# Kernel tuning notes

Hardware: AMD Instinct MI355X
Metric: run time of the kernel (lower is better)

Reference implementation:

```python
import jax, jax.numpy as jnp
import numpy as np

B, S, D, H = 4, 2048, 1024, 16
HD = D // H  # head_dim = 64


def setup_inputs() -> dict:
    key = jax.random.key(0)
    ks = jax.random.split(key, 6)
    scale = 0.02
    x = jax.random.normal(ks[0], (B, S, D), dtype=jnp.float32)
    # per-head projection weights, torch Linear is y = x @ W.T; store as [H, D, HD]
    Wq = jax.random.normal(ks[1], (H, D, HD), dtype=jnp.float32) * scale
    Wk = jax.random.normal(ks[2], (H, D, HD), dtype=jnp.float32) * scale
    Wv = jax.random.normal(ks[3], (H, D, HD), dtype=jnp.float32) * scale
    Wo = jax.random.normal(ks[4], (D, D), dtype=jnp.float32) * scale  # torch [out, in]
    bo = jax.random.normal(ks[5], (D,), dtype=jnp.float32) * scale
    return {"x": x, "Wq": Wq, "Wk": Wk, "Wv": Wv, "Wo": Wo, "bo": bo}


def reference(x, Wq, Wk, Wv, Wo, bo):
    # project: [B,S,D] x [H,D,HD] -> [B,H,S,HD]
    q = jnp.einsum("bsd,hde->bhse", x, Wq)
    k = jnp.einsum("bsd,hde->bhse", x, Wk)
    v = jnp.einsum("bsd,hde->bhse", x, Wv)
    scores = jnp.einsum("bhse,bhte->bhst", q, k) / jnp.sqrt(jnp.float32(HD))
    causal = jnp.tril(jnp.ones((S, S), dtype=bool))  # same as registered tril mask
    scores = jnp.where(causal, scores, -jnp.inf)
    w = jax.nn.softmax(scores, axis=-1)
    out = jnp.einsum("bhst,bhte->bhse", w, v)  # [B,H,S,HD]
    # concat heads along feature dim: [B,S,H*HD] = [B,S,D]
    out = out.transpose(0, 2, 1, 3).reshape(B, S, D)
    # output projection: torch Linear y = x @ W.T + b
    return jnp.einsum("bsd,od->bso", out, Wo) + bo
```

## Files before the change

kernel.cpp:

```cpp
#include <hip/hip_runtime.h>
#include <hip/hip_bf16.h>

typedef __bf16 bf16x8 __attribute__((ext_vector_type(8)));
typedef float f32x4 __attribute__((ext_vector_type(4)));
typedef unsigned short u16x4 __attribute__((ext_vector_type(4)));
typedef unsigned short u16x8 __attribute__((ext_vector_type(8)));
typedef unsigned uint4v __attribute__((ext_vector_type(4)));

#define B_ 4
#define S_ 2048
#define D_ 1024
#define H_ 16
#define HD_ 64

__device__ __forceinline__ unsigned short f2bf(float f) {
  unsigned u = __float_as_uint(f);
  u += 0x7fff + ((u >> 16) & 1);
  return (unsigned short)(u >> 16);
}

__device__ __forceinline__ void gload16(const void* g, void* l) {
  __builtin_amdgcn_global_load_lds((const __attribute__((address_space(1))) unsigned int*)g,
                                   (__attribute__((address_space(3))) unsigned int*)l,
                                   16, 0, 0);
}

__global__ void pack_x_k(const float* __restrict__ in, unsigned short* __restrict__ out, int n4) {
  int i = blockIdx.x * blockDim.x + threadIdx.x;
  int stride = gridDim.x * blockDim.x;
  for (; i < n4; i += stride) {
    float4 v = reinterpret_cast<const float4*>(in)[i];
    u16x4 o = {f2bf(v.x), f2bf(v.y), f2bf(v.z), f2bf(v.w)};
    reinterpret_cast<u16x4*>(out)[i] = o;
  }
}

__global__ void pack_wqkv_k(const float* __restrict__ Wq, const float* __restrict__ Wk,
                            const float* __restrict__ Wv, unsigned short* __restrict__ Wt) {
  int o = blockIdx.x * blockDim.x + threadIdx.x;
  int n = o >> 10;
  int d = o & 1023;
  const float* W = (n < 1024) ? Wq : (n < 2048) ? Wk : Wv;
  int nn = n & 1023;
  int h = nn >> 6, e = nn & 63;
  Wt[o] = f2bf(W[(h << 16) + (d << 6) + e]);
}

__global__ __launch_bounds__(512, 2) void gemm256_k(const unsigned short* __restrict__ A,
                                                    const unsigned short* __restrict__ Bt,
                                                    unsigned short* __restrict__ QK,
                                                    unsigned short* __restrict__ VT,
                                                    int M, int N, int K) {
  __shared__ __align__(16) unsigned short lA0[2][128 * 64];
  __shared__ __align__(16) unsigned short lA1[2][128 * 64];
  __shared__ __align__(16) unsigned short lB[2][192 * 64];
  const int tid = threadIdx.x;
  const int wid = tid >> 6, lane = tid & 63;
  const int r = lane & 15, g = lane >> 4;
  const int wm = wid >> 2, wn = wid & 3;

  const int i_hw = blockIdx.y * gridDim.x + blockIdx.x;
  const int xcd = i_hw & 7, j = i_hw >> 3;
  const long arow0 = (long)((xcd & 3) * 8 + (j & 7)) * 256;
  const long bcol0 = (long)((xcd >> 2) * 8 + (j >> 3)) * 192;

  const f32x4 z4 = {0.f, 0.f, 0.f, 0.f};
  f32x4 acc[8][3];
#pragma unroll
  for (int m = 0; m < 8; ++m)
#pragma unroll
    for (int n = 0; n < 3; ++n) acc[m][n] = z4;

  auto stage_half = [&](int kt, int which) {
    const unsigned short* src = (which == 2) ? Bt + bcol0 * K : A + (arow0 + 128 * which) * K;
    const int k0 = kt << 6;
    unsigned short* base = (which == 0) ? &lA0[kt & 1][0]
                         : (which == 1) ? &lA1[kt & 1][0] : &lB[kt & 1][0];
    const int nch = (which == 2) ? 3 : 2;
    for (int c = 0; c < nch; ++c) {
      const int jj = c * 512 + tid;
      const int row = jj >> 3, cc = jj & 7;
      const int ccs = cc ^ (row & 7);
      gload16(src + (long)row * K + k0 + ccs * 8, base + jj * 8);
    }
  };

  bf16x8 af[4][2], bv[3][2];
  auto read_a = [&](const unsigned short* lbase) {
#pragma unroll
    for (int i2 = 0; i2 < 4; ++i2)
#pragma unroll
      for (int kk = 0; kk < 2; ++kk) {
        const int rowh = (2 * i2 + wm) * 16 + r;
        af[i2][kk] = *(const bf16x8*)&lbase[rowh * 64 + (((kk << 2) + g) ^ (rowh & 7)) * 8];
      }
  };
  auto read_b = [&](int buf) {
#pragma unroll
    for (int j2 = 0; j2 < 3; ++j2)
#pragma unroll
      for (int kk = 0; kk < 2; ++kk) {
        const int rowh = (4 * j2 + wn) * 16 + r;
        bv[j2][kk] = *(const bf16x8*)&lB[buf][rowh * 64 + (((kk << 2) + g) ^ (rowh & 7)) * 8];
      }
  };
  auto mma_h = [&](int mh) {
    __builtin_amdgcn_s_setprio(1);
#pragma unroll
    for (int kk = 0; kk < 2; ++kk)
#pragma unroll
      for (int i2 = 0; i2 < 4; ++i2)
#pragma unroll
        for (int j2 = 0; j2 < 3; ++j2)
          acc[4 * mh + i2][j2] = __builtin_amdgcn_mfma_f32_16x16x32_bf16(
              af[i2][kk], bv[j2][kk], acc[4 * mh + i2][j2], 0, 0, 0);
    __builtin_amdgcn_s_setprio(0);
  };

  const int nk = K >> 6;
  stage_half(0, 0);
  stage_half(0, 2);
  stage_half(0, 1);
  asm volatile("s_waitcnt vmcnt(2)" ::: "memory");
  asm volatile("s_barrier" ::: "memory");

  for (int t = 0; t < nk; ++t) {
    const int buf = t & 1;
    const bool pre = (t + 1 < nk);
    read_a(&lA0[buf][0]);
    read_b(buf);
    if (pre) { stage_half(t + 1, 0); stage_half(t + 1, 2); }
    asm volatile("s_barrier" ::: "memory");
    mma_h(0);
    if (pre) asm volatile("s_waitcnt vmcnt(5)" ::: "memory");
    else     asm volatile("s_waitcnt vmcnt(0)" ::: "memory");
    asm volatile("s_waitcnt lgkmcnt(0)\n\ts_barrier" ::: "memory");
    read_a(&lA1[buf][0]);
    if (pre) stage_half(t + 1, 1);
    asm volatile("s_barrier" ::: "memory");
    mma_h(1);
    if (pre) asm volatile("s_waitcnt vmcnt(2)" ::: "memory");
    asm volatile("s_waitcnt lgkmcnt(0)\n\ts_barrier" ::: "memory");
  }

#pragma unroll
  for (int j2 = 0; j2 < 3; ++j2) {
    const long colb = bcol0 + (4 * j2 + wn) * 16;
    if (colb < 2048) {
#pragma unroll
      for (int m = 0; m < 8; ++m)
#pragma unroll
        for (int rr = 0; rr < 4; ++rr) {
          const long row = arow0 + (2 * m + wm) * 16 + g * 4 + rr;
          QK[row * 2048 + colb + r] = f2bf(acc[m][j2][rr]);
        }
    } else {
      const long vcol = colb - 2048 + r;
      const long h = vcol >> 6, e = vcol & 63;
#pragma unroll
      for (int m = 0; m < 8; ++m) {
        const long row0 = arow0 + (2 * m + wm) * 16 + g * 4;
        const long b = row0 >> 11, s = row0 & 2047;
        u16x4 w4;
#pragma unroll
        for (int rr = 0; rr < 4; ++rr) w4[rr] = f2bf(acc[m][j2][rr]);
        *(u16x4*)&VT[(((b << 4) + h) * 64 + e) * 2048 + s] = w4;
      }
    }
  }
}

__global__ __launch_bounds__(512, 2) void gemm_op_k(const unsigned short* __restrict__ A,
                                                    const unsigned short* __restrict__ Bt,
                                                    float* __restrict__ C,
                                                    const float* __restrict__ bias,
                                                    int M, int N, int K) {
  __shared__ __align__(16) unsigned short lA0[2][128 * 64];
  __shared__ __align__(16) unsigned short lA1[2][128 * 64];
  __shared__ __align__(16) unsigned short lB[2][128 * 64];
  const int tid = threadIdx.x;
  const int wid = tid >> 6, lane = tid & 63;
  const int r = lane & 15, g = lane >> 4;
  const int wm = wid >> 2, wn = wid & 3;

  const int i_hw = blockIdx.y * gridDim.x + blockIdx.x;
  const int xcd = i_hw & 7, j = i_hw >> 3;
  const long arow0 = (long)((xcd & 3) * 8 + (j & 7)) * 256;
  const long bcol0 = (long)((xcd >> 2) * 4 + (j >> 3)) * 128;

  const f32x4 z4 = {0.f, 0.f, 0.f, 0.f};
  f32x4 acc[8][2];
#pragma unroll
  for (int m = 0; m < 8; ++m)
#pragma unroll
    for (int n = 0; n < 2; ++n) acc[m][n] = z4;

  auto stage_half = [&](int kt, int which) {
    const unsigned short* src = (which == 2) ? Bt + bcol0 * K : A + (arow0 + 128 * which) * K;
    const int k0 = kt << 6;
    unsigned short* base = (which == 0) ? &lA0[kt & 1][0]
                         : (which == 1) ? &lA1[kt & 1][0] : &lB[kt & 1][0];
#pragma unroll
    for (int c = 0; c < 2; ++c) {
      const int jj = c * 512 + tid;
      const int row = jj >> 3, cc = jj & 7;
      const int ccs = cc ^ (row & 7);
      gload16(src + (long)row * K + k0 + ccs * 8, base + jj * 8);
    }
  };

  bf16x8 af[4][2], bv[2][2];
  auto read_a = [&](const unsigned short* lbase) {
#pragma unroll
    for (int i2 = 0; i2 < 4; ++i2)
#pragma unroll
      for (int kk = 0; kk < 2; ++kk) {
        const int rowh = (2 * i2 + wm) * 16 + r;
        af[i2][kk] = *(const bf16x8*)&lbase[rowh * 64 + (((kk << 2) + g) ^ (rowh & 7)) * 8];
      }
  };
  auto read_b = [&](int buf) {
#pragma unroll
    for (int j2 = 0; j2 < 2; ++j2)
#pragma unroll
      for (int kk = 0; kk < 2; ++kk) {
        const int rowh = (4 * j2 + wn) * 16 + r;
        bv[j2][kk] = *(const bf16x8*)&lB[buf][rowh * 64 + (((kk << 2) + g) ^ (rowh & 7)) * 8];
      }
  };
  auto mma_h = [&](int mh) {
    __builtin_amdgcn_s_setprio(1);
#pragma unroll
    for (int kk = 0; kk < 2; ++kk)
#pragma unroll
      for (int i2 = 0; i2 < 4; ++i2)
#pragma unroll
        for (int j2 = 0; j2 < 2; ++j2)
          acc[4 * mh + i2][j2] = __builtin_amdgcn_mfma_f32_16x16x32_bf16(
              af[i2][kk], bv[j2][kk], acc[4 * mh + i2][j2], 0, 0, 0);
    __builtin_amdgcn_s_setprio(0);
  };

  const int nk = K >> 6;
  stage_half(0, 0);
  stage_half(0, 2);
  stage_half(0, 1);
  asm volatile("s_waitcnt vmcnt(2)" ::: "memory");
  asm volatile("s_barrier" ::: "memory");

  for (int t = 0; t < nk; ++t) {
    const int buf = t & 1;
    const bool pre = (t + 1 < nk);
    read_a(&lA0[buf][0]);
    read_b(buf);
    if (pre) { stage_half(t + 1, 0); stage_half(t + 1, 2); }
    asm volatile("s_barrier" ::: "memory");
    mma_h(0);
    if (pre) asm volatile("s_waitcnt vmcnt(4)" ::: "memory");
    else     asm volatile("s_waitcnt vmcnt(0)" ::: "memory");
    asm volatile("s_waitcnt lgkmcnt(0)\n\ts_barrier" ::: "memory");
    read_a(&lA1[buf][0]);
    if (pre) stage_half(t + 1, 1);
    asm volatile("s_barrier" ::: "memory");
    mma_h(1);
    if (pre) asm volatile("s_waitcnt vmcnt(2)" ::: "memory");
    asm volatile("s_waitcnt lgkmcnt(0)\n\ts_barrier" ::: "memory");
  }

#pragma unroll
  for (int m = 0; m < 8; ++m)
#pragma unroll
    for (int n = 0; n < 2; ++n)
#pragma unroll
      for (int rr = 0; rr < 4; ++rr) {
        const long row = arow0 + (2 * m + wm) * 16 + g * 4 + rr;
        const long col = bcol0 + (4 * n + wn) * 16 + r;
        C[row * N + col] = acc[m][n][rr] + bias[col];
      }
}

__global__ __launch_bounds__(256, 2) void attn_k(const unsigned short* __restrict__ qk,
                                                 const unsigned short* __restrict__ vt,
                                                 unsigned short* __restrict__ out) {
  __shared__ __align__(16) unsigned short lK[2][64 * 64];
  __shared__ __align__(16) unsigned short lVt[2][64 * 64];

  const int tid = threadIdx.x, wid = tid >> 6, lane = tid & 63;
  const int r = lane & 15, g = lane >> 4;
  const int bh = blockIdx.x;
  const int b = bh >> 4, h = bh & 15;
  const int qb = 15 - (int)blockIdx.y;
  const int q0 = qb * 128;

  const unsigned short* Qg = qk + ((long)b * S_) * 2048 + h * 64;
  const unsigned short* Kg = Qg + 1024;
  const unsigned short* Vg = vt + ((long)(b * 16 + h)) * 64 * 2048;

  int qrow[2];
  bf16x8 qf[2][2];
#pragma unroll
  for (int qs = 0; qs < 2; ++qs) {
    qrow[qs] = q0 + qs * 64 + wid * 16 + r;
#pragma unroll
    for (int kk = 0; kk < 2; ++kk)
      qf[qs][kk] = *(const bf16x8*)&Qg[(long)qrow[qs] * 2048 + kk * 32 + g * 8];
  }

  const f32x4 z4 = {0.f, 0.f, 0.f, 0.f};
  f32x4 o[2][4];
#pragma unroll
  for (int qs = 0; qs < 2; ++qs)
#pragma unroll
    for (int nt = 0; nt < 4; ++nt) o[qs][nt] = z4;
  float m_i[2] = {-1e30f, -1e30f};
  float l_i[2] = {0.f, 0.f};

  auto stage = [&](int buf, int t0) {
#pragma unroll
    for (int c = 0; c < 2; ++c) {
      const int j = c * 256 + tid;
      const int row = j >> 3, cc = j & 7;
      const int ccs = (cc ^ (row & 7)) << 3;
      gload16(Kg + (long)(t0 + row) * 2048 + ccs, &lK[buf][j * 8]);
      gload16(Vg + (long)row * 2048 + t0 + ccs, &lVt[buf][j * 8]);
    }
  };

  const int ntiles = (q0 >> 6) + 2;
  stage(0, 0);

  for (int t = 0; t < ntiles; ++t) {
    const int cur = t & 1;
    __syncthreads();
    if (t + 1 < ntiles) stage(cur ^ 1, (t + 1) << 6);

    const int t0 = t << 6;
    const bool act0 = (t < ntiles - 1);
    const bool diag0 = (t == ntiles - 2);
    const bool diag1 = (t == ntiles - 1);

    f32x4 st[2][4];
#pragma unroll
    for (int tt = 0; tt < 4; ++tt) { st[0][tt] = z4; st[1][tt] = z4; }
    __builtin_amdgcn_s_setprio(1);
#pragma unroll
    for (int kk = 0; kk < 2; ++kk)
#pragma unroll
      for (int tt = 0; tt < 4; ++tt) {
        const int row = tt * 16 + r, cc = kk * 4 + g;
        bf16x8 kf = *(const bf16x8*)&lK[cur][(row * 8 + (cc ^ (row & 7))) * 8];
        st[1][tt] = __builtin_amdgcn_mfma_f32_16x16x32_bf16(kf, qf[1][kk], st[1][tt], 0, 0, 0);
        if (act0)
          st[0][tt] = __builtin_amdgcn_mfma_f32_16x16x32_bf16(kf, qf[0][kk], st[0][tt], 0, 0, 0);
      }
    __builtin_amdgcn_s_setprio(0);

    bf16x8 pf[2][2];
    unsigned corr_bits[2] = {0x3f800000u, 0x3f800000u};
    bool dodef[2] = {true, true};
#pragma unroll
    for (int qs = 0; qs < 2; ++qs) {
      if (qs == 0 && !act0) continue;
      const bool diag = qs ? diag1 : diag0;
      float sv[16];
#pragma unroll
      for (int tt = 0; tt < 4; ++tt)
#pragma unroll
        for (int rg = 0; rg < 4; ++rg) {
          float s = st[qs][tt][rg];
          if (diag && (t0 + tt * 16 + g * 4 + rg > qrow[qs])) s = -1e30f;
          sv[tt * 4 + rg] = s;
        }
      float h0 = fmaxf(fmaxf(fmaxf(sv[0], sv[1]), fmaxf(sv[2], sv[3])),
                       fmaxf(fmaxf(sv[4], sv[5]), fmaxf(sv[6], sv[7])));
      float h1 = fmaxf(fmaxf(fmaxf(sv[8], sv[9]), fmaxf(sv[10], sv[11])),
                       fmaxf(fmaxf(sv[12], sv[13]), fmaxf(sv[14], sv[15])));
      const float pmax = fmaxf(h0, h1);
      const bool defer = __all(pmax - m_i[qs] <= 64.f);
      float corr = 1.f;
      if (!defer) {
        float mx = fmaxf(pmax, m_i[qs]);
        mx = fmaxf(mx, __shfl_xor(mx, 16, 64));
        mx = fmaxf(mx, __shfl_xor(mx, 32, 64));
        corr = __expf((m_i[qs] - mx) * 0.125f);
        m_i[qs] = mx;
      }
      dodef[qs] = defer;
      corr_bits[qs] = __float_as_uint(corr);
      const float m8 = m_i[qs] * 0.125f;
      float p[16];
      float rs = 0.f;
#pragma unroll
      for (int i = 0; i < 16; ++i) {
        p[i] = __expf(__builtin_fmaf(sv[i], 0.125f, -m8));
        rs += p[i];
      }
      rs += __shfl_xor(rs, 16, 64);
      rs += __shfl_xor(rs, 32, 64);
      l_i[qs] = l_i[qs] * corr + rs;
      unsigned cw[4][2];
#pragma unroll
      for (int tt = 0; tt < 4; ++tt)
#pragma unroll
        for (int e = 0; e < 2; ++e)
          asm("v_cvt_pk_bf16_f32 %0, %1, %2"
              : "=v"(cw[tt][e]) : "v"(p[tt * 4 + 2 * e]), "v"(p[tt * 4 + 2 * e + 1]));
#pragma unroll
      for (int kk = 0; kk < 2; ++kk) {
        unsigned x0 = cw[2 * kk][0], y0 = cw[2 * kk + 1][0];
        unsigned x1 = cw[2 * kk][1], y1 = cw[2 * kk + 1][1];
        asm volatile("v_permlane32_swap_b32 %0, %1" : "+v"(x0), "+v"(y0));
        asm volatile("v_permlane16_swap_b32 %0, %1" : "+v"(x0), "+v"(y0));
        asm volatile("v_permlane32_swap_b32 %0, %1" : "+v"(x1), "+v"(y1));
        asm volatile("v_permlane16_swap_b32 %0, %1" : "+v"(x1), "+v"(y1));
        uint4v w = {x0, x1, y0, y1};
        pf[qs][kk] = *(bf16x8*)&w;
      }
    }
#pragma unroll
    for (int qs = 0; qs < 2; ++qs) {
      if (qs == 0 && !act0) continue;
      if (!dodef[qs]) {
        const float corr = __uint_as_float(corr_bits[qs]);
#pragma unroll
        for (int rr = 0; rr < 4; ++rr) {
          const float c = __shfl(corr, g * 4 + rr, 64);
#pragma unroll
          for (int nt = 0; nt < 4; ++nt) o[qs][nt][rr] *= c;
        }
      }
    }

    __builtin_amdgcn_s_setprio(1);
#pragma unroll
    for (int kk = 0; kk < 2; ++kk)
#pragma unroll
      for (int nt = 0; nt < 4; ++nt) {
        const int row = nt * 16 + r, cc = kk * 4 + g;
        const bf16x8 vf = *(const bf16x8*)&lVt[cur][(row * 8 + (cc ^ (row & 7))) * 8];
        o[1][nt] = __builtin_amdgcn_mfma_f32_16x16x32_bf16(pf[1][kk], vf, o[1][nt], 0, 0, 0);
        if (act0)
          o[0][nt] = __builtin_amdgcn_mfma_f32_16x16x32_bf16(pf[0][kk], vf, o[0][nt], 0, 0, 0);
      }
    __builtin_amdgcn_s_setprio(0);
  }

#pragma unroll
  for (int qs = 0; qs < 2; ++qs) {
    float linv[4];
#pragma unroll
    for (int rr = 0; rr < 4; ++rr)
      linv[rr] = 1.f / __shfl(l_i[qs], g * 4 + rr, 64);
#pragma unroll
    for (int nt = 0; nt < 4; ++nt)
#pragma unroll
      for (int rr = 0; rr < 4; ++rr) {
        const long s = q0 + qs * 64 + wid * 16 + g * 4 + rr;
        out[((long)b * S_ + s) * 1024 + h * 64 + nt * 16 + r] = f2bf(o[qs][nt][rr] * linv[rr]);
      }
  }
}

extern "C" void kernel_launch(void* const* d_in, const int* in_sizes, int n_in,
                              void* d_out, int out_size, void* d_ws, size_t ws_size,
                              hipStream_t stream) {
  const float* x = (const float*)d_in[0];
  const float* Wq = (const float*)d_in[1];
  const float* Wk = (const float*)d_in[2];
  const float* Wv = (const float*)d_in[3];
  const float* Wo = (const float*)d_in[4];
  const float* bo = (const float*)d_in[5];
  float* out = (float*)d_out;

  char* ws = (char*)d_ws;
  unsigned short* Xb = (unsigned short*)(ws);
  unsigned short* Wt = (unsigned short*)(ws + (16ul << 20));
  unsigned short* Wob = (unsigned short*)(ws + (22ul << 20));
  unsigned short* QK = (unsigned short*)(ws + (24ul << 20));
  unsigned short* VT = (unsigned short*)(ws + (56ul << 20));
  unsigned short* AO = (unsigned short*)(ws + (72ul << 20));

  pack_x_k<<<2048, 256, 0, stream>>>(x, Xb, (B_ * S_ * D_) / 4);
  pack_x_k<<<512, 256, 0, stream>>>(Wo, Wob, (D_ * D_) / 4);
  pack_wqkv_k<<<(3 * D_ * D_) / 256, 256, 0, stream>>>(Wq, Wk, Wv, Wt);

  gemm256_k<<<dim3(32, 16), 512, 0, stream>>>(Xb, Wt, QK, VT, B_ * S_, 3 * D_, D_);
  attn_k<<<dim3(64, 16), 256, 0, stream>>>(QK, VT, AO);
  gemm_op_k<<<dim3(32, 8), 512, 0, stream>>>(AO, Wob, out, bo, B_ * S_, D_, D_);
}
```

Before: 178.8 us.

## Widen attention KV tiles from 64 to 128 keys per iteration

Each attention loop iteration now stages and processes 128 keys instead of 64, doubling the K and V^T LDS buffers and widening the V swizzle to 16 chunks. This halves the number of iterations, barriers and online-softmax max/sum reductions per query block. Both query sub-tiles now run for every tile, with masking applied only on the final diagonal tile. The cost is more LDS (64KB per block, which may limit occupancy to 2 blocks per CU), more registers for scores and probabilities, and some extra MFMA work on masked diagonal regions.

```diff
diff --git a/kernel.cpp b/kernel.cpp
--- a/kernel.cpp
+++ b/kernel.cpp
@@ -282,8 +282,8 @@
 __global__ __launch_bounds__(256, 2) void attn_k(const unsigned short* __restrict__ qk,
                                                  const unsigned short* __restrict__ vt,
                                                  unsigned short* __restrict__ out) {
-  __shared__ __align__(16) unsigned short lK[2][64 * 64];
-  __shared__ __align__(16) unsigned short lVt[2][64 * 64];
+  __shared__ __align__(16) unsigned short lK[2][128 * 64];
+  __shared__ __align__(16) unsigned short lVt[2][64 * 128];
 
   const int tid = threadIdx.x, wid = tid >> 6, lane = tid & 63;
   const int r = lane & 15, g = lane >> 4;
@@ -317,65 +317,70 @@
 
   auto stage = [&](int buf, int t0) {
 #pragma unroll
-    for (int c = 0; c < 2; ++c) {
+    for (int c = 0; c < 4; ++c) {
       const int j = c * 256 + tid;
       const int row = j >> 3, cc = j & 7;
       const int ccs = (cc ^ (row & 7)) << 3;
       gload16(Kg + (long)(t0 + row) * 2048 + ccs, &lK[buf][j * 8]);
-      gload16(Vg + (long)row * 2048 + t0 + ccs, &lVt[buf][j * 8]);
-    }
-  };
-
-  const int ntiles = (q0 >> 6) + 2;
+      const int vrow = j >> 4, vcc = j & 15;
+      const int vccs = (vcc ^ (vrow & 15)) << 3;
+      gload16(Vg + (long)vrow * 2048 + t0 + vccs, &lVt[buf][j * 8]);
+    }
+  };
+
+  const int ntiles = qb + 1;
   stage(0, 0);
 
   for (int t = 0; t < ntiles; ++t) {
     const int cur = t & 1;
     __syncthreads();
-    if (t + 1 < ntiles) stage(cur ^ 1, (t + 1) << 6);
-
-    const int t0 = t << 6;
-    const bool act0 = (t < ntiles - 1);
-    const bool diag0 = (t == ntiles - 2);
-    const bool diag1 = (t == ntiles - 1);
-
-    f32x4 st[2][4];
-#pragma unroll
-    for (int tt = 0; tt < 4; ++tt) { st[0][tt] = z4; st[1][tt] = z4; }
+    if (t + 1 < ntiles) stage(cur ^ 1, (t + 1) << 7);
+
+    const int t0 = t << 7;
+    const bool diag = (t == ntiles - 1);
+
+    f32x4 st[2][8];
+#pragma unroll
+    for (int tt = 0; tt < 8; ++tt) { st[0][tt] = z4; st[1][tt] = z4; }
     __builtin_amdgcn_s_setprio(1);
 #pragma unroll
     for (int kk = 0; kk < 2; ++kk)
 #pragma unroll
-      for (int tt = 0; tt < 4; ++tt) {
+      for (int tt = 0; tt < 8; ++tt) {
         const int row = tt * 16 + r, cc = kk * 4 + g;
         bf16x8 kf = *(const bf16x8*)&lK[cur][(row * 8 + (cc ^ (row & 7))) * 8];
         st[1][tt] = __builtin_amdgcn_mfma_f32_16x16x32_bf16(kf, qf[1][kk], st[1][tt], 0, 0, 0);
-        if (act0)
-          st[0][tt] = __builtin_amdgcn_mfma_f32_16x16x32_bf16(kf, qf[0][kk], st[0][tt], 0, 0, 0);
+        st[0][tt] = __builtin_amdgcn_mfma_f32_16x16x32_bf16(kf, qf[0][kk], st[0][tt], 0, 0, 0);
       }
     __builtin_amdgcn_s_setprio(0);
 
-    bf16x8 pf[2][2];
+    bf16x8 pf[2][4];
     unsigned corr_bits[2] = {0x3f800000u, 0x3f800000u};
     bool dodef[2] = {true, true};
 #pragma unroll
     for (int qs = 0; qs < 2; ++qs) {
-      if (qs == 0 && !act0) continue;
-      const bool diag = qs ? diag1 : diag0;
-      float sv[16];
-#pragma unroll
-      for (int tt = 0; tt < 4; ++tt)
-#pragma unroll
-        for (int rg = 0; rg < 4; ++rg) {
-          float s = st[qs][tt][rg];
-          if (diag && (t0 + tt * 16 + g * 4 + rg > qrow[qs])) s = -1e30f;
-          sv[tt * 4 + rg] = s;
-        }
-      float h0 = fmaxf(fmaxf(fmaxf(sv[0], sv[1]), fmaxf(sv[2], sv[3])),
-                       fmaxf(fmaxf(sv[4], sv[5]), fmaxf(sv[6], sv[7])));
-      float h1 = fmaxf(fmaxf(fmaxf(sv[8], sv[9]), fmaxf(sv[10], sv[11])),
-                       fmaxf(fmaxf(sv[12], sv[13]), fmaxf(sv[14], sv[15])));
-      const float pmax = fmaxf(h0, h1);
+      float sv[32];
+      if (diag) {
+#pragma unroll
+        for (int tt = 0; tt < 8; ++tt)
+#pragma unroll
+          for (int rg = 0; rg < 4; ++rg) {
+            float s = st[qs][tt][rg];
+            if (t0 + tt * 16 + g * 4 + rg > qrow[qs]) s = -1e30f;
+            sv[tt * 4 + rg] = s;
+          }
+      } else {
+#pragma unroll
+        for (int tt = 0; tt < 8; ++tt)
+#pragma unroll
+          for (int rg = 0; rg < 4; ++rg) sv[tt * 4 + rg] = st[qs][tt][rg];
+      }
+      float hx[4];
+#pragma unroll
+      for (int q4 = 0; q4 < 4; ++q4)
+        hx[q4] = fmaxf(fmaxf(fmaxf(sv[q4 * 8], sv[q4 * 8 + 1]), fmaxf(sv[q4 * 8 + 2], sv[q4 * 8 + 3])),
+                       fmaxf(fmaxf(sv[q4 * 8 + 4], sv[q4 * 8 + 5]), fmaxf(sv[q4 * 8 + 6], sv[q4 * 8 + 7])));
+      const float pmax = fmaxf(fmaxf(hx[0], hx[1]), fmaxf(hx[2], hx[3]));
       const bool defer = __all(pmax - m_i[qs] <= 64.f);
       float corr = 1.f;
       if (!defer) {
@@ -388,25 +393,25 @@
       dodef[qs] = defer;
       corr_bits[qs] = __float_as_uint(corr);
       const float m8 = m_i[qs] * 0.125f;
-      float p[16];
+      float p[32];
       float rs = 0.f;
 #pragma unroll
-      for (int i = 0; i < 16; ++i) {
+      for (int i = 0; i < 32; ++i) {
         p[i] = __expf(__builtin_fmaf(sv[i], 0.125f, -m8));
         rs += p[i];
       }
       rs += __shfl_xor(rs, 16, 64);
       rs += __shfl_xor(rs, 32, 64);
       l_i[qs] = l_i[qs] * corr + rs;
-      unsigned cw[4][2];
-#pragma unroll
-      for (int tt = 0; tt < 4; ++tt)
+      unsigned cw[8][2];
+#pragma unroll
+      for (int tt = 0; tt < 8; ++tt)
 #pragma unroll
         for (int e = 0; e < 2; ++e)
           asm("v_cvt_pk_bf16_f32 %0, %1, %2"
               : "=v"(cw[tt][e]) : "v"(p[tt * 4 + 2 * e]), "v"(p[tt * 4 + 2 * e + 1]));
 #pragma unroll
-      for (int kk = 0; kk < 2; ++kk) {
+      for (int kk = 0; kk < 4; ++kk) {
         unsigned x0 = cw[2 * kk][0], y0 = cw[2 * kk + 1][0];
         unsigned x1 = cw[2 * kk][1], y1 = cw[2 * kk + 1][1];
         asm volatile("v_permlane32_swap_b32 %0, %1" : "+v"(x0), "+v"(y0));
@@ -419,7 +424,6 @@
     }
 #pragma unroll
     for (int qs = 0; qs < 2; ++qs) {
-      if (qs == 0 && !act0) continue;
       if (!dodef[qs]) {
         const float corr = __uint_as_float(corr_bits[qs]);
 #pragma unroll
@@ -433,14 +437,13 @@
 
     __builtin_amdgcn_s_setprio(1);
 #pragma unroll
-    for (int kk = 0; kk < 2; ++kk)
+    for (int kk = 0; kk < 4; ++kk)
 #pragma unroll
       for (int nt = 0; nt < 4; ++nt) {
-        const int row = nt * 16 + r, cc = kk * 4 + g;
-        const bf16x8 vf = *(const bf16x8*)&lVt[cur][(row * 8 + (cc ^ (row & 7))) * 8];
+        const int row = nt * 16 + r;
+        const bf16x8 vf = *(const bf16x8*)&lVt[cur][row * 128 + (((kk * 4 + g) ^ r)) * 8];
         o[1][nt] = __builtin_amdgcn_mfma_f32_16x16x32_bf16(pf[1][kk], vf, o[1][nt], 0, 0, 0);
-        if (act0)
-          o[0][nt] = __builtin_amdgcn_mfma_f32_16x16x32_bf16(pf[0][kk], vf, o[0][nt], 0, 0, 0);
+        o[0][nt] = __builtin_amdgcn_mfma_f32_16x16x32_bf16(pf[0][kk], vf, o[0][nt], 0, 0, 0);
       }
     __builtin_amdgcn_s_setprio(0);
   }
```

Result: no change. 178.9 us (+0.1%).
